# Optimization experiments

Measured on AMD Instinct MI355X. Metric: run time of the kernel, lower is better.

## Reference

```python
import jax, jax.numpy as jnp
import numpy as np

D_MODEL = 512
D_FFN = 1024
B, N = 8, 2048


def setup_inputs() -> dict:
    key = jax.random.key(0)
    k1, k2, k3, k4, k5, k6 = jax.random.split(key, 6)
    x = jax.random.normal(k1, (B, N, D_MODEL), dtype=jnp.float32)
    interaction_mask = jax.random.randint(k2, (B, N, N), 0, 2).astype(jnp.float32)
    s1 = 1.0 / np.sqrt(D_MODEL)
    s2 = 1.0 / np.sqrt(D_FFN)
    W1 = jax.random.uniform(k3, (D_MODEL, D_FFN), jnp.float32, -s1, s1)
    b1 = jax.random.uniform(k4, (D_FFN,), jnp.float32, -s1, s1)
    W2 = jax.random.uniform(k5, (D_FFN, 3 * D_MODEL), jnp.float32, -s2, s2)
    b2 = jax.random.uniform(k6, (3 * D_MODEL,), jnp.float32, -s2, s2)
    return {"x": x, "interaction_mask": interaction_mask,
            "W1": W1, "b1": b1, "W2": W2, "b2": b2}


def reference(x, interaction_mask, W1, b1, W2, b2):
    # 2-layer FFN: Linear -> ReLU -> Linear (identity)
    h = jax.nn.relu(x @ W1 + b1)           # [B, N, d_ffn]
    kqv = h @ W2 + b2                        # [B, N, 3*d_model]
    k, q, v = jnp.split(kqv, 3, axis=-1)     # each [B, N, d_model]
    scale = D_MODEL ** -0.5
    # softmax-free scaled dot-product
    attn = jnp.einsum("bqd,bkd->bqk", q, k) * scale  # [B, N, N]
    attn = attn * interaction_mask
    return jnp.einsum("bqk,bkd->bqd", attn, v)        # [B, N, d_model]
```

## Files before the change

### kernel.cpp

```cpp
#include <hip/hip_runtime.h>
#include <hip/hip_bf16.h>

typedef __attribute__((ext_vector_type(8))) short bf16x8;
typedef __attribute__((ext_vector_type(4))) float f32x4;

#define NB 8
#define NN 2048
#define DM 512
#define DF 1024

__device__ __forceinline__ ushort f2b(float f) {
  union { __hip_bfloat16 h; ushort u; } c;
  c.h = __float2bfloat16(f);
  return c.u;
}
__device__ __forceinline__ float b2f(ushort u) {
  union { ushort u; __hip_bfloat16 h; } c;
  c.u = u;
  return __bfloat162float(c.h);
}

typedef __attribute__((address_space(1))) const void gvoid_t;
typedef __attribute__((address_space(3))) void svoid_t;
__device__ __forceinline__ void gload16(const void* g, void* s) {
  __builtin_amdgcn_global_load_lds((gvoid_t*)g, (svoid_t*)s, 16, 0, 0);
}

__device__ __forceinline__ void gemm_core_128(
    const ushort* __restrict__ A, const ushort* __restrict__ B,
    int K, int brow, int bcol, f32x4 (&acc)[4][4], ushort* smem)
{
  const int tid = threadIdx.x;
  const int w = tid >> 6, l = tid & 63;
  const int sr = (w << 3) + (l >> 3);
  const int sc = (((l & 7) ^ (l >> 3)) << 3);
  const int fr = l & 15;
  const int arow = ((w >> 1) << 6) + fr;
  const int brw  = ((w & 1) << 6) + fr;
  char* base = (char*)smem;
  char* A0 = base;          char* B0 = base + 16384;
  char* A1 = base + 32768;  char* B1 = base + 49152;

#pragma unroll
  for (int m = 0; m < 4; m++)
#pragma unroll
    for (int n = 0; n < 4; n++)
      acc[m][n] = (f32x4){0.f, 0.f, 0.f, 0.f};

  const ushort* Ap = A + (long)(brow + sr) * K + sc;
  const ushort* Bp = B + (long)(bcol + sr) * K + sc;
  const int nkt = K >> 6;

  auto stage = [&](char* Ad, char* Bd, int kt) {
#pragma unroll
    for (int i = 0; i < 4; i++) {
      gload16(Ap + (long)i * 32 * K + kt * 64, Ad + i * 4096 + (w << 10));
      gload16(Bp + (long)i * 32 * K + kt * 64, Bd + i * 4096 + (w << 10));
    }
  };
  auto compute = [&](const char* As_, const char* Bs_) {
#pragma unroll
    for (int kk = 0; kk < 2; kk++) {
      const int cx = ((((kk << 2) + (l >> 4)) ^ (l & 7)) << 4);
      bf16x8 a[4], b[4];
#pragma unroll
      for (int m = 0; m < 4; m++)
        a[m] = *(const bf16x8*)(As_ + (arow + m * 16) * 128 + cx);
#pragma unroll
      for (int n = 0; n < 4; n++)
        b[n] = *(const bf16x8*)(Bs_ + (brw + n * 16) * 128 + cx);
#pragma unroll
      for (int m = 0; m < 4; m++)
#pragma unroll
        for (int n = 0; n < 4; n++)
          acc[m][n] = __builtin_amdgcn_mfma_f32_16x16x32_bf16(a[m], b[n], acc[m][n], 0, 0, 0);
    }
  };

  stage(A0, B0, 0);
  __syncthreads();
  for (int kt = 0; kt < nkt; kt += 2) {
    stage(A1, B1, kt + 1);
    compute(A0, B0);
    __syncthreads();
    if (kt + 2 < nkt) stage(A0, B0, kt + 2);
    compute(A1, B1);
    __syncthreads();
  }
}

__device__ __forceinline__ void acc_to_lds_bf16(f32x4 (&acc)[4][4], ushort* smem) {
  const int tid = threadIdx.x, w = tid >> 6, l = tid & 63;
  const int r0l = ((w >> 1) << 6) + ((l >> 4) << 2);
  const int c0l = ((w & 1) << 6) + (l & 15);
#pragma unroll
  for (int n = 0; n < 4; n++)
#pragma unroll
    for (int m = 0; m < 4; m++)
#pragma unroll
      for (int j = 0; j < 4; j++)
        smem[(r0l + m * 16 + j) * 128 + (c0l + n * 16)] = f2b(acc[m][n][j]);
}


__global__ __launch_bounds__(256) void k_cvt(const float* __restrict__ in,
                                             ushort* __restrict__ out) {
  const long i = ((long)blockIdx.x * 256 + threadIdx.x) << 2;
  const float4 v = *(const float4*)(in + i);
  ushort4 o;
  o.x = f2b(v.x); o.y = f2b(v.y); o.z = f2b(v.z); o.w = f2b(v.w);
  *(ushort4*)(out + i) = o;
}

__global__ __launch_bounds__(256) void k_trw(const float* __restrict__ in, ushort* __restrict__ out,
                                             int R, int C) {
  __shared__ float t[32][33];
  const int c0 = blockIdx.x << 5, r0 = blockIdx.y << 5;
  const int tx = threadIdx.x & 31, ty = threadIdx.x >> 5;
#pragma unroll
  for (int j = 0; j < 32; j += 8)
    t[ty + j][tx] = in[(long)(r0 + ty + j) * C + (c0 + tx)];
  __syncthreads();
#pragma unroll
  for (int j = 0; j < 32; j += 8)
    out[(long)(c0 + ty + j) * R + (r0 + tx)] = f2b(t[tx][ty + j]);
}

__global__ __launch_bounds__(256) void k_gemm1(const ushort* __restrict__ xb,
                                               const ushort* __restrict__ w1t,
                                               const float* __restrict__ b1,
                                               ushort* __restrict__ hb) {
  __shared__ ushort smem[128 * 256];
  f32x4 acc[4][4];
  const int brow = blockIdx.x << 7, bcol = blockIdx.y << 7;
  gemm_core_128(xb, w1t, DM, brow, bcol, acc, smem);
  const int tid = threadIdx.x, w = tid >> 6, l = tid & 63;
  const int c0l = ((w & 1) << 6) + (l & 15);
#pragma unroll
  for (int n = 0; n < 4; n++) {
    const float bias = b1[bcol + c0l + n * 16];
#pragma unroll
    for (int m = 0; m < 4; m++)
#pragma unroll
      for (int j = 0; j < 4; j++) {
        float v = acc[m][n][j] + bias;
        acc[m][n][j] = v > 0.f ? v : 0.f;
      }
  }
  acc_to_lds_bf16(acc, smem);
  __syncthreads();
  const int rb = tid >> 4, cb = tid & 15;
#pragma unroll
  for (int i = 0; i < 8; i++) {
    const int row = i * 16 + rb;
    bf16x8 s = *(const bf16x8*)(smem + row * 128 + cb * 8);
    *(bf16x8*)(hb + (long)(brow + row) * DF + bcol + cb * 8) = s;
  }
}

__global__ __launch_bounds__(256) void k_gemm2(const ushort* __restrict__ hb,
                                               const ushort* __restrict__ w2t,
                                               const float* __restrict__ b2,
                                               ushort* __restrict__ kb,
                                               ushort* __restrict__ qb,
                                               ushort* __restrict__ vtb) {
  __shared__ ushort smem[128 * 256];
  f32x4 acc[4][4];
  const int brow = blockIdx.x << 7, bcol = blockIdx.y << 7;
  gemm_core_128(hb, w2t, DF, brow, bcol, acc, smem);
  const int seg = bcol >> 9;
  const float sc = (seg == 1) ? 0.04419417382415922f : 1.0f;
  const int tid = threadIdx.x, w = tid >> 6, l = tid & 63;
  const int c0l = ((w & 1) << 6) + (l & 15);
#pragma unroll
  for (int n = 0; n < 4; n++) {
    const float bias = b2[bcol + c0l + n * 16];
#pragma unroll
    for (int m = 0; m < 4; m++)
#pragma unroll
      for (int j = 0; j < 4; j++)
        acc[m][n][j] = (acc[m][n][j] + bias) * sc;
  }
  acc_to_lds_bf16(acc, smem);
  __syncthreads();
  const int clb = bcol - (seg << 9);
  if (seg < 2) {
    ushort* dst = (seg == 0) ? kb : qb;
    const int rb = tid >> 4, cb = tid & 15;
#pragma unroll
    for (int i = 0; i < 8; i++) {
      const int row = i * 16 + rb;
      bf16x8 s = *(const bf16x8*)(smem + row * 128 + cb * 8);
      *(bf16x8*)(dst + (long)(brow + row) * DM + clb + cb * 8) = s;
    }
  } else {
    const int batch = brow >> 11;
    const int rbase = brow & 2047;
    const int c = tid & 127, rc = tid >> 7;
    ushort* vt = vtb + (long)batch * DM * NN + (long)(clb + c) * NN + rbase;
#pragma unroll
    for (int it = 0; it < 8; ++it) {
      const int chunk = rc * 8 + it;
      bf16x8 o;
#pragma unroll
      for (int j = 0; j < 8; ++j)
        o[j] = (short)smem[(chunk * 8 + j) * 128 + c];
      *(bf16x8*)(vt + chunk * 8) = o;
    }
  }
}

__global__ __launch_bounds__(512) void k_qk(const ushort* __restrict__ qb,
                                            const ushort* __restrict__ kb,
                                            const float* __restrict__ mask,
                                            ushort* __restrict__ Sbuf) {
  __shared__ ushort smem[24576];
  const int bid = blockIdx.x;
  const int batch = bid & 7;
  const int t = bid >> 3;
  const int brow = (t & 7) << 8;
  const int bcol = (t >> 3) << 7;
  const ushort* A = qb + (long)batch * NN * DM;
  const ushort* B = kb + (long)batch * NN * DM;
  const float* mk = mask + (long)batch * NN * NN;
  ushort* S = Sbuf + (long)batch * NN * NN;

  const int tid = threadIdx.x;
  const int w = tid >> 6, l = tid & 63;
  const int wr = w & 3, wc = w >> 2;
  const int fr = l & 15;
  char* AsB = (char*)smem;
  char* BsB = AsB + 32768;

  f32x4 acc[4][4];
#pragma unroll
  for (int m = 0; m < 4; m++)
#pragma unroll
    for (int n = 0; n < 4; n++)
      acc[m][n] = (f32x4){0.f, 0.f, 0.f, 0.f};

  const int srow = (w << 3) + (l >> 3);
  const int sc = (((l & 7) ^ (l >> 3)) << 3);
  const ushort* Ap = A + (long)(brow + srow) * DM + sc;
  const ushort* Bp = B + (long)(bcol + srow) * DM + sc;

  for (int kt = 0; kt < 8; ++kt) {
#pragma unroll
    for (int i = 0; i < 4; i++)
      gload16(Ap + (long)i * 64 * DM + kt * 64, AsB + i * 8192 + (w << 10));
#pragma unroll
    for (int i = 0; i < 2; i++)
      gload16(Bp + (long)i * 64 * DM + kt * 64, BsB + i * 8192 + (w << 10));
    __syncthreads();
#pragma unroll
    for (int kk = 0; kk < 2; kk++) {
      const int cx = ((((kk << 2) + (l >> 4)) ^ (l & 7)) << 4);
      bf16x8 b[4], a[4];
#pragma unroll
      for (int n = 0; n < 4; n++)
        b[n] = *(const bf16x8*)(BsB + ((wc << 6) + (n << 4) + fr) * 128 + cx);
#pragma unroll
      for (int m = 0; m < 4; m++)
        a[m] = *(const bf16x8*)(AsB + ((wr << 6) + (m << 4) + fr) * 128 + cx);
#pragma unroll
      for (int m = 0; m < 4; m++)
#pragma unroll
        for (int n = 0; n < 4; n++)
          acc[m][n] = __builtin_amdgcn_mfma_f32_16x16x32_bf16(a[m], b[n], acc[m][n], 0, 0, 0);
    }
    __syncthreads();
  }

  const int rb = tid >> 4, cb = tid & 15;
#pragma unroll
  for (int h = 0; h < 2; ++h) {
    if ((wr >> 1) == h) {
      const int r0l = ((wr & 1) << 6) + ((l >> 4) << 2);
      const int c0l = (wc << 6) + fr;
#pragma unroll
      for (int n = 0; n < 4; n++)
#pragma unroll
        for (int m = 0; m < 4; m++)
#pragma unroll
          for (int j = 0; j < 4; j++)
            smem[(r0l + m * 16 + j) * 128 + (c0l + n * 16)] = f2b(acc[m][n][j]);
    }
    __syncthreads();
#pragma unroll
    for (int i = 0; i < 4; i++) {
      const int row = i * 32 + rb;
      const long goff = (long)(brow + h * 128 + row) * NN + bcol + cb * 8;
      bf16x8 s = *(const bf16x8*)(smem + row * 128 + cb * 8);
      const f32x4 m0 = __builtin_nontemporal_load((const f32x4*)(mk + goff));
      const f32x4 m1 = __builtin_nontemporal_load((const f32x4*)(mk + goff + 4));
      bf16x8 o;
      o[0] = (short)f2b(b2f((ushort)s[0]) * m0[0]);
      o[1] = (short)f2b(b2f((ushort)s[1]) * m0[1]);
      o[2] = (short)f2b(b2f((ushort)s[2]) * m0[2]);
      o[3] = (short)f2b(b2f((ushort)s[3]) * m0[3]);
      o[4] = (short)f2b(b2f((ushort)s[4]) * m1[0]);
      o[5] = (short)f2b(b2f((ushort)s[5]) * m1[1]);
      o[6] = (short)f2b(b2f((ushort)s[6]) * m1[2]);
      o[7] = (short)f2b(b2f((ushort)s[7]) * m1[3]);
      *(bf16x8*)(S + goff) = o;
    }
    __syncthreads();
  }
}

__global__ __launch_bounds__(256) void k_pv(const ushort* __restrict__ Sbuf,
                                            const ushort* __restrict__ vtb,
                                            float* __restrict__ out) {
  __shared__ ushort smem[128 * 256];
  const int bid = blockIdx.x;
  const int batch = bid & 7;
  const int t = bid >> 3;
  const int brow = (t & 15) << 7;
  const int bcol = (t >> 4) << 7;
  const ushort* A = Sbuf + (long)batch * NN * NN;
  const ushort* Bm = vtb + (long)batch * DM * NN;
  float* op = out + (long)batch * NN * DM;
  f32x4 acc[4][4];
  gemm_core_128(A, Bm, NN, brow, bcol, acc, smem);
  float* fs = (float*)smem;
  const int tid = threadIdx.x, w = tid >> 6, l = tid & 63;
  const int r0l = ((w >> 1) << 6) + ((l >> 4) << 2);
  const int c0l = ((w & 1) << 6) + (l & 15);
#pragma unroll
  for (int n = 0; n < 4; n++)
#pragma unroll
    for (int m = 0; m < 4; m++)
#pragma unroll
      for (int j = 0; j < 4; j++)
        fs[(r0l + m * 16 + j) * 128 + (c0l + n * 16)] = acc[m][n][j];
  __syncthreads();
  const int rg = tid >> 5, l32 = tid & 31;
#pragma unroll
  for (int p = 0; p < 16; ++p) {
    const int row = p * 8 + rg;
    const float4 v = *(const float4*)(fs + row * 128 + l32 * 4);
    *(float4*)(op + (long)(brow + row) * DM + bcol + l32 * 4) = v;
  }
}

extern "C" void kernel_launch(void* const* d_in, const int* in_sizes, int n_in,
                              void* d_out, int out_size, void* d_ws, size_t ws_size,
                              hipStream_t stream) {
  const float* x    = (const float*)d_in[0];
  const float* mask = (const float*)d_in[1];
  const float* W1   = (const float*)d_in[2];
  const float* b1   = (const float*)d_in[3];
  const float* W2   = (const float*)d_in[4];
  const float* b2   = (const float*)d_in[5];
  float* out = (float*)d_out;

  char* ws = (char*)d_ws;
  size_t off = 0;
  auto alloc = [&](size_t n) { char* p = ws + off; off += (n + 255) & ~(size_t)255; return p; };
  ushort* xb  = (ushort*)alloc((size_t)NB * NN * DM * 2);
  ushort* hb  = (ushort*)alloc((size_t)NB * NN * DF * 2);
  ushort* w1t = (ushort*)alloc((size_t)DF * DM * 2);
  ushort* w2t = (ushort*)alloc((size_t)3 * DM * DF * 2);
  ushort* kb  = (ushort*)alloc((size_t)NB * NN * DM * 2);
  ushort* qb  = (ushort*)alloc((size_t)NB * NN * DM * 2);
  ushort* vtb = (ushort*)alloc((size_t)NB * NN * DM * 2);
  ushort* Sbuf = (ushort*)alloc((size_t)NB * NN * NN * 2);

  k_cvt<<<dim3(8192), dim3(256), 0, stream>>>(x, xb);
  k_trw<<<dim3(DF / 32, DM / 32), dim3(256), 0, stream>>>(W1, w1t, DM, DF);
  k_trw<<<dim3(3 * DM / 32, DF / 32), dim3(256), 0, stream>>>(W2, w2t, DF, 3 * DM);
  k_gemm1<<<dim3(NB * NN / 128, DF / 128), dim3(256), 0, stream>>>(xb, w1t, b1, hb);
  k_gemm2<<<dim3(NB * NN / 128, 3 * DM / 128), dim3(256), 0, stream>>>(hb, w2t, b2, kb, qb, vtb);
  k_qk<<<dim3(1024), dim3(512), 0, stream>>>(qb, kb, mask, Sbuf);
  k_pv<<<dim3(512), dim3(256), 0, stream>>>(Sbuf, vtb, out);
}
```

Before: 211.9 us.

## Triple-buffer QK^T tile loads with async prefetch two k-steps ahead

Replaces the single-buffered load-sync-compute loop in the QK^T kernel with a three-stage LDS ring buffer. Global-to-LDS loads for tile kt+2 are issued in halves, interleaved with the MFMA work on tile kt, and guarded by explicit vmcnt waits and barriers. The MFMA block also runs at raised wave priority. This is meant to hide global memory latency behind compute, at the cost of raising LDS use to 144KB per block, which lowers occupancy and makes correctness depend on hand-placed waitcnt and barrier logic.

```diff
diff --git a/kernel.cpp b/kernel.cpp
--- a/kernel.cpp
+++ b/kernel.cpp
@@ -214,7 +214,7 @@
                                             const ushort* __restrict__ kb,
                                             const float* __restrict__ mask,
                                             ushort* __restrict__ Sbuf) {
-  __shared__ ushort smem[24576];
+  __shared__ ushort smem[73728];
   const int bid = blockIdx.x;
   const int batch = bid & 7;
   const int t = bid >> 3;
@@ -229,8 +229,7 @@
   const int w = tid >> 6, l = tid & 63;
   const int wr = w & 3, wc = w >> 2;
   const int fr = l & 15;
-  char* AsB = (char*)smem;
-  char* BsB = AsB + 32768;
+  char* base = (char*)smem;
 
   f32x4 acc[4][4];
 #pragma unroll
@@ -241,34 +240,63 @@
 
   const int srow = (w << 3) + (l >> 3);
   const int sc = (((l & 7) ^ (l >> 3)) << 3);
-  const ushort* Ap = A + (long)(brow + srow) * DM + sc;
-  const ushort* Bp = B + (long)(bcol + srow) * DM + sc;
-
+
+  auto stage_chunk = [&](int b, int kt, int c) {
+    if (c < 4)
+      gload16(A + (long)(brow + (c << 6) + srow) * DM + (kt << 6) + sc,
+              base + b * 49152 + (c << 13) + (w << 10));
+    else
+      gload16(B + (long)(bcol + ((c - 4) << 6) + srow) * DM + (kt << 6) + sc,
+              base + b * 49152 + 32768 + ((c - 4) << 13) + (w << 10));
+  };
+  auto stage_tile = [&](int b, int kt) {
+#pragma unroll
+    for (int c = 0; c < 6; ++c) stage_chunk(b, kt, c);
+  };
+
+  stage_tile(0, 0);
+  stage_tile(1, 1);
+  asm volatile("s_waitcnt vmcnt(6)" ::: "memory");
+  __builtin_amdgcn_s_barrier();
+
+#pragma unroll
   for (int kt = 0; kt < 8; ++kt) {
-#pragma unroll
-    for (int i = 0; i < 4; i++)
-      gload16(Ap + (long)i * 64 * DM + kt * 64, AsB + i * 8192 + (w << 10));
-#pragma unroll
-    for (int i = 0; i < 2; i++)
-      gload16(Bp + (long)i * 64 * DM + kt * 64, BsB + i * 8192 + (w << 10));
-    __syncthreads();
-#pragma unroll
-    for (int kk = 0; kk < 2; kk++) {
+    const int b = kt % 3;
+    const char* AsB = base + b * 49152;
+    const char* BsB = AsB + 32768;
+#pragma unroll
+    for (int kk = 0; kk < 2; ++kk) {
       const int cx = ((((kk << 2) + (l >> 4)) ^ (l & 7)) << 4);
-      bf16x8 b[4], a[4];
+      bf16x8 bfr[4], a[4];
 #pragma unroll
       for (int n = 0; n < 4; n++)
-        b[n] = *(const bf16x8*)(BsB + ((wc << 6) + (n << 4) + fr) * 128 + cx);
+        bfr[n] = *(const bf16x8*)(BsB + ((wc << 6) + (n << 4) + fr) * 128 + cx);
 #pragma unroll
       for (int m = 0; m < 4; m++)
         a[m] = *(const bf16x8*)(AsB + ((wr << 6) + (m << 4) + fr) * 128 + cx);
+      if (kt + 2 < 8) {
+        const int b2 = (kt + 2) % 3;
+#pragma unroll
+        for (int c = 0; c < 3; ++c) stage_chunk(b2, kt + 2, kk * 3 + c);
+      }
+      __builtin_amdgcn_s_barrier();
+      asm volatile("s_waitcnt lgkmcnt(0)" ::: "memory");
+      __builtin_amdgcn_sched_barrier(0);
+      __builtin_amdgcn_s_setprio(1);
 #pragma unroll
       for (int m = 0; m < 4; m++)
 #pragma unroll
         for (int n = 0; n < 4; n++)
-          acc[m][n] = __builtin_amdgcn_mfma_f32_16x16x32_bf16(a[m], b[n], acc[m][n], 0, 0, 0);
-    }
-    __syncthreads();
+          acc[m][n] = __builtin_amdgcn_mfma_f32_16x16x32_bf16(a[m], bfr[n], acc[m][n], 0, 0, 0);
+      __builtin_amdgcn_s_setprio(0);
+      if (kk == 1) {
+        if (kt + 2 < 8)
+          asm volatile("s_waitcnt vmcnt(6)" ::: "memory");
+        else if (kt + 1 < 8)
+          asm volatile("s_waitcnt vmcnt(0)" ::: "memory");
+      }
+      __builtin_amdgcn_s_barrier();
+    }
   }
 
   const int rb = tid >> 4, cb = tid & 15;
```

New measurement: 219.6 us. +3.6%, slower.
